# Performance work log

Measured on AMD Instinct MI355X. Metric: run time of the kernel, lower is better.

## Reference

```python
import jax, jax.numpy as jnp
import numpy as np

N_NODES = 100000
N_EDGES = 1600000
EMB = 64       # embedding_dim
HID = 128      # hidden_channels
N_GRAPHS = 512
N_TASKS = 128
ATOM_VOCAB = 119
BOND_VOCAB = 16


def setup_inputs() -> dict:
    key = jax.random.key(0)
    ks = jax.random.split(key, 24)
    s = 0.02
    inp = {
        'x_idx': jax.random.randint(ks[0], (N_NODES,), 0, ATOM_VOCAB),
        'edge_index': jax.random.randint(ks[1], (2, N_EDGES), 0, N_NODES),
        'edge_attr_idx': jax.random.randint(ks[2], (N_EDGES,), 0, BOND_VOCAB),
        'batch': jnp.sort(jax.random.randint(ks[3], (N_NODES,), 0, N_GRAPHS)),
        'atom_emb': jax.random.normal(ks[4], (ATOM_VOCAB, EMB), jnp.float32) * s,
        'bond_emb': jax.random.normal(ks[5], (BOND_VOCAB, EMB), jnp.float32) * s,
        'w_edge0': jax.random.normal(ks[6], (EMB, EMB), jnp.float32) * s,
        'b_edge0': jnp.zeros((EMB,), jnp.float32),
        'w1_0': jax.random.normal(ks[7], (EMB, HID), jnp.float32) * s,
        'b1_0': jnp.zeros((HID,), jnp.float32),
        'w2_0': jax.random.normal(ks[8], (HID, HID), jnp.float32) * s,
        'b2_0': jnp.zeros((HID,), jnp.float32),
        'w_edge1': jax.random.normal(ks[9], (EMB, HID), jnp.float32) * s,
        'b_edge1': jnp.zeros((HID,), jnp.float32),
        'w1_1': jax.random.normal(ks[10], (HID, HID), jnp.float32) * s,
        'b1_1': jnp.zeros((HID,), jnp.float32),
        'w2_1': jax.random.normal(ks[11], (HID, HID), jnp.float32) * s,
        'b2_1': jnp.zeros((HID,), jnp.float32),
        'lin1_w': jax.random.normal(ks[12], (HID, HID), jnp.float32) * s,
        'lin1_b': jnp.zeros((HID,), jnp.float32),
        'lin2_w': jax.random.normal(ks[13], (HID, N_TASKS), jnp.float32) * s,
        'lin2_b': jnp.zeros((N_TASKS,), jnp.float32),
    }
    return inp


def _gine_conv(x, e, src, dst, we, be, w1, b1, w2, b2):
    # message: relu(x_j + Linear(edge_attr)); aggregate: scatter-add at dst
    msg = jax.nn.relu(x[src] + e @ we + be)            # [E, in_dim]
    agg = jax.ops.segment_sum(msg, dst, num_segments=N_NODES)
    h = x + agg                                        # (1+eps)*x with eps=0
    h = jax.nn.elu(h @ w1 + b1) @ w2 + b2              # GINE nn MLP
    return jax.nn.elu(h)                               # outer F.elu


def reference(x_idx, edge_index, edge_attr_idx, batch,
              atom_emb, bond_emb,
              w_edge0, b_edge0, w1_0, b1_0, w2_0, b2_0,
              w_edge1, b_edge1, w1_1, b1_1, w2_1, b2_1,
              lin1_w, lin1_b, lin2_w, lin2_b):
    x = atom_emb[x_idx]                                # [N, EMB]
    e = bond_emb[edge_attr_idx]                        # [E, EMB]
    src, dst = edge_index[0], edge_index[1]            # flow: source->target
    x = _gine_conv(x, e, src, dst, w_edge0, b_edge0, w1_0, b1_0, w2_0, b2_0)
    x = _gine_conv(x, e, src, dst, w_edge1, b_edge1, w1_1, b1_1, w2_1, b2_1)
    hg = jax.ops.segment_sum(x, batch, num_segments=N_GRAPHS)  # global_add_pool
    hg = jax.nn.relu(hg @ lin1_w + lin1_b)
    return hg @ lin2_w + lin2_b                        # [G, num_tasks]
```

## Files before the change

### kernel.cpp

```cpp
#include <hip/hip_runtime.h>
#include <hip/hip_bf16.h>

static const int NN = 100000;
static const int NE = 1600000;
static const int NG = 512;
static const int NB = 391;
static const int PS = 4608;
static const int CS = 4624;

typedef __attribute__((ext_vector_type(8))) short shortx8;
typedef __attribute__((ext_vector_type(4))) float floatx4;
typedef __attribute__((ext_vector_type(2))) float floatx2;

__device__ __forceinline__ float bf2f(unsigned short u) {
  union { unsigned int i; float f; } v; v.i = ((unsigned int)u) << 16; return v.f;
}
__device__ __forceinline__ unsigned short f2bf(float f) {
  union { float f; unsigned int i; } v; v.f = f;
  return (unsigned short)((v.i + 0x7FFFu + ((v.i >> 16) & 1u)) >> 16);
}
__device__ __forceinline__ float elu_fast(float v) {
  return v > 0.f ? v : (__builtin_amdgcn_exp2f(v * 1.44269504f) - 1.f);
}
__device__ __forceinline__ floatx2 unpk(unsigned int v) {
  union { unsigned int i; float f; } a, b;
  a.i = v << 16; b.i = v & 0xFFFF0000u;
  floatx2 r; r.x = a.f; r.y = b.f; return r;
}

__global__ void k_prep(const float* __restrict__ bond,
                       const float* __restrict__ we0, const float* __restrict__ be0,
                       const float* __restrict__ we1, const float* __restrict__ be1,
                       const float* __restrict__ atom,
                       float* __restrict__ et1, unsigned short* __restrict__ M0,
                       float* __restrict__ hgf, int* __restrict__ bcursor,
                       const float* __restrict__ s0, const float* __restrict__ s1,
                       const float* __restrict__ s2, const float* __restrict__ s3,
                       const float* __restrict__ s4, const float* __restrict__ s5,
                       unsigned short* __restrict__ d0, unsigned short* __restrict__ d1,
                       unsigned short* __restrict__ d2, unsigned short* __restrict__ d3,
                       unsigned short* __restrict__ d4, unsigned short* __restrict__ d5) {
  int blk = blockIdx.x, t = threadIdx.x;
  if (blk < 8) {
    int i = blk * 256 + t;
    int b = i >> 7, c = i & 127;
    float acc = be1[c];
    for (int k = 0; k < 64; ++k) acc += bond[b * 64 + k] * we1[k * 128 + c];
    et1[i] = acc;
  } else if (blk < 484) {
    int i = (blk - 8) * 256 + t;
    int c = i & 63, b = (i >> 6) & 15, a = i >> 10;
    float acc = be0[c];
    for (int k = 0; k < 64; ++k) acc += bond[b * 64 + k] * we0[k * 64 + c];
    acc += atom[a * 64 + c];
    M0[i] = f2bf(acc > 0.f ? acc : 0.f);
  } else if (blk < 868) {
    int task = (blk - 484) >> 6;
    int i = ((blk - 484) & 63) * 256 + t;
    const float* w; unsigned short* wz; int K;
    switch (task) {
      case 0: w = s0; wz = d0; K = 64; break;
      case 1: w = s1; wz = d1; K = 128; break;
      case 2: w = s2; wz = d2; K = 128; break;
      case 3: w = s3; wz = d3; K = 128; break;
      case 4: w = s4; wz = d4; K = 128; break;
      default: w = s5; wz = d5; K = 128; break;
    }
    if (i >= K * 128) return;
    int j = i & 7, lane = (i >> 3) & 63, ct = (i >> 9) & 7, s = i >> 12;
    int k = s * 32 + (lane >> 4) * 8 + j;
    int m = ct * 16 + (lane & 15);
    wz[i] = f2bf(w[k * 128 + m]);
  } else if (blk < 884) {
    int base = (blk - 868) * 4096;
#pragma unroll
    for (int k = 0; k < 16; ++k) hgf[base + k * 256 + t] = 0.f;
  } else {
    if (t < NB) bcursor[t] = t * PS;
    int u = t + 256;
    if (u < NB) bcursor[u] = u * PS;
  }
}

__global__ void k_bin(const int* __restrict__ src, const int* __restrict__ dstp,
                      const int* __restrict__ ea, const int* __restrict__ x_idx,
                      int* __restrict__ bcursor, uint2* __restrict__ pairs) {
  __shared__ int cnt[512];
  __shared__ int incl[512];
  __shared__ int cur[NB];
  __shared__ int rbase[NB];
  __shared__ uint2 stage[2048];
  int t = threadIdx.x;
  int e0 = blockIdx.x * 2048;
  int ecnt = NE - e0; if (ecnt > 2048) ecnt = 2048;
  cnt[t] = 0; cnt[t + 256] = 0;
  __syncthreads();
  for (int k = 0; k < 8; ++k) {
    int i = k * 256 + t;
    if (i < ecnt) atomicAdd(&cnt[dstp[e0 + i] >> 8], 1);
  }
  __syncthreads();
  incl[t] = cnt[t]; incl[t + 256] = cnt[t + 256];
  __syncthreads();
  for (int d = 1; d < 512; d <<= 1) {
    int v0 = (t >= d) ? incl[t - d] : 0;
    int v1 = (t + 256 >= d) ? incl[t + 256 - d] : 0;
    __syncthreads();
    incl[t] += v0; incl[t + 256] += v1;
    __syncthreads();
  }
  if (t < NB) { cur[t] = incl[t] - cnt[t]; if (cnt[t]) rbase[t] = atomicAdd(&bcursor[t], cnt[t]); }
  int u = t + 256;
  if (u < NB) { cur[u] = incl[u] - cnt[u]; if (cnt[u]) rbase[u] = atomicAdd(&bcursor[u], cnt[u]); }
  __syncthreads();
  for (int k = 0; k < 8; ++k) {
    int i = k * 256 + t;
    if (i < ecnt) {
      int e = e0 + i;
      int d = dstp[e];
      int s = src[e];
      unsigned int pk = (unsigned int)s | ((unsigned int)(x_idx[s] * 16 + ea[e]) << 17);
      int p = atomicAdd(&cur[d >> 8], 1);
      stage[p] = make_uint2((unsigned int)d, pk);
    }
  }
  __syncthreads();
  for (int j = t; j < ecnt; j += 256) {
    uint2 p = stage[j];
    int b = (int)(p.x >> 8);
    int excl = incl[b] - cnt[b];
    pairs[rbase[b] + (j - excl)] = p;
  }
}

__global__ void k_fine(const uint2* __restrict__ pairs, const int* __restrict__ bcursor,
                       int* __restrict__ offs, int* __restrict__ cnts,
                       unsigned int* __restrict__ csr0, unsigned int* __restrict__ csr1) {
  __shared__ int cnt[256];
  __shared__ int incl[256];
  __shared__ int cur[256];
  int b = blockIdx.x;
  int t = threadIdx.x;
  int start = b * PS;
  int endv = bcursor[b];
  int cbase = b * CS;
  int base_n = b << 8;
  cnt[t] = 0;
  __syncthreads();
  for (int j = start + t; j < endv; j += 256)
    atomicAdd(&cnt[(int)pairs[j].x - base_n], 1);
  __syncthreads();
  incl[t] = cnt[t];
  __syncthreads();
  for (int d = 1; d < 256; d <<= 1) {
    int v = (t >= d) ? incl[t - d] : 0;
    __syncthreads();
    incl[t] += v;
    __syncthreads();
  }
  int excl = incl[t] - cnt[t];
  cur[t] = excl;
  int node = base_n + t;
  if (node < NN) { offs[node] = cbase + excl; cnts[node] = cnt[t]; }
  __syncthreads();
  for (int j = start + t; j < endv; j += 256) {
    uint2 p = pairs[j];
    int pos = cbase + atomicAdd(&cur[(int)p.x - base_n], 1);
    unsigned int pk = p.y;
    unsigned int idx17 = pk >> 17;
    csr0[pos] = idx17 << 7;
    csr1[pos] = ((pk & 0x1FFFFu) << 8) | (idx17 & 15u);
  }
  __syncthreads();
  int total = incl[255];
  if (t < 16) { csr0[cbase + total + t] = 0u; csr1[cbase + total + t] = 0u; }
}

__global__ __launch_bounds__(256) void k_agg0(
    const int* __restrict__ x_idx, const float* __restrict__ atom,
    const unsigned short* __restrict__ M0, const int* __restrict__ offs,
    const int* __restrict__ cnts,
    const unsigned int* __restrict__ csr0, unsigned short* __restrict__ h0) {
  int t = threadIdx.x, lane = t & 63;
  int half = lane >> 5, c = lane & 31;
  int n = __builtin_amdgcn_readfirstlane(blockIdx.x * 4 + (t >> 6));
  if (n >= NN) return;
  int s = offs[n], e = s + cnts[n];
  const char* Mb = (const char*)M0;
  unsigned int voff = (unsigned int)c * 4u;
  floatx2 acc; acc.x = 0.f; acc.y = 0.f;
  if (half == 0) {
    float2 sv = *(const float2*)((const char*)atom +
                                 ((size_t)(unsigned)x_idx[n] << 8) + (size_t)c * 8u);
    acc.x = sv.x; acc.y = sv.y;
  }
  for (int i = s; i < e; i += 16) {
    unsigned int a0 = csr0[i + 0],  b0 = csr0[i + 1];
    unsigned int a1 = csr0[i + 2],  b1 = csr0[i + 3];
    unsigned int a2 = csr0[i + 4],  b2 = csr0[i + 5];
    unsigned int a3 = csr0[i + 6],  b3 = csr0[i + 7];
    unsigned int a4 = csr0[i + 8],  b4 = csr0[i + 9];
    unsigned int a5 = csr0[i + 10], b5 = csr0[i + 11];
    unsigned int a6 = csr0[i + 12], b6 = csr0[i + 13];
    unsigned int a7 = csr0[i + 14], b7 = csr0[i + 15];
    unsigned int q0 = half ? b0 : a0, q1 = half ? b1 : a1;
    unsigned int q2 = half ? b2 : a2, q3 = half ? b3 : a3;
    unsigned int q4 = half ? b4 : a4, q5 = half ? b5 : a5;
    unsigned int q6 = half ? b6 : a6, q7 = half ? b7 : a7;
    floatx2 m0, m1, m2, m3, m4, m5, m6, m7;
    m0.x = m0.y = (i + 0 + half < e) ? 1.f : 0.f;
    m1.x = m1.y = (i + 2 + half < e) ? 1.f : 0.f;
    m2.x = m2.y = (i + 4 + half < e) ? 1.f : 0.f;
    m3.x = m3.y = (i + 6 + half < e) ? 1.f : 0.f;
    m4.x = m4.y = (i + 8 + half < e) ? 1.f : 0.f;
    m5.x = m5.y = (i + 10 + half < e) ? 1.f : 0.f;
    m6.x = m6.y = (i + 12 + half < e) ? 1.f : 0.f;
    m7.x = m7.y = (i + 14 + half < e) ? 1.f : 0.f;
    unsigned int v0 = *(const unsigned int*)(Mb + q0 + voff);
    unsigned int v1 = *(const unsigned int*)(Mb + q1 + voff);
    unsigned int v2 = *(const unsigned int*)(Mb + q2 + voff);
    unsigned int v3 = *(const unsigned int*)(Mb + q3 + voff);
    unsigned int v4 = *(const unsigned int*)(Mb + q4 + voff);
    unsigned int v5 = *(const unsigned int*)(Mb + q5 + voff);
    unsigned int v6 = *(const unsigned int*)(Mb + q6 + voff);
    unsigned int v7 = *(const unsigned int*)(Mb + q7 + voff);
    acc = __builtin_elementwise_fma(m0, unpk(v0), acc);
    acc = __builtin_elementwise_fma(m1, unpk(v1), acc);
    acc = __builtin_elementwise_fma(m2, unpk(v2), acc);
    acc = __builtin_elementwise_fma(m3, unpk(v3), acc);
    acc = __builtin_elementwise_fma(m4, unpk(v4), acc);
    acc = __builtin_elementwise_fma(m5, unpk(v5), acc);
    acc = __builtin_elementwise_fma(m6, unpk(v6), acc);
    acc = __builtin_elementwise_fma(m7, unpk(v7), acc);
  }
  float ax = acc.x + __shfl_xor(acc.x, 32);
  float ay = acc.y + __shfl_xor(acc.y, 32);
  if (half == 0) {
    unsigned int o = (unsigned int)f2bf(ax) | ((unsigned int)f2bf(ay) << 16);
    *(unsigned int*)(h0 + (size_t)n * 64 + c * 2) = o;
  }
}

__global__ __launch_bounds__(256) void k_agg1(
    const unsigned short* __restrict__ x1, const float* __restrict__ et1,
    const int* __restrict__ offs, const int* __restrict__ cnts,
    const unsigned int* __restrict__ csr1, unsigned short* __restrict__ h1) {
  __shared__ float etl[2048];
  int t = threadIdx.x;
#pragma unroll
  for (int k = 0; k < 8; ++k) etl[k * 256 + t] = et1[k * 256 + t];
  __syncthreads();
  int lane = t & 63;
  int n = __builtin_amdgcn_readfirstlane(blockIdx.x * 4 + (t >> 6));
  if (n >= NN) return;
  int s = offs[n], e = s + cnts[n];
  const char* xb = (const char*)x1;
  unsigned int voff = (unsigned int)lane * 4u;
  const char* etb = (const char*)etl + (size_t)lane * 8u;
  unsigned int xv = *(const unsigned int*)(xb + ((size_t)(unsigned)n << 8) + voff);
  floatx2 acc = unpk(xv);
  floatx2 zero2; zero2.x = 0.f; zero2.y = 0.f;
  for (int i = s; i < e; i += 8) {
    unsigned int q0 = csr1[i + 0], q1 = csr1[i + 1], q2 = csr1[i + 2], q3 = csr1[i + 3];
    unsigned int q4 = csr1[i + 4], q5 = csr1[i + 5], q6 = csr1[i + 6], q7 = csr1[i + 7];
    floatx2 k1, k2, k3, k4, k5, k6, k7;
    k1.x = k1.y = (i + 1 < e) ? 1.f : 0.f;
    k2.x = k2.y = (i + 2 < e) ? 1.f : 0.f;
    k3.x = k3.y = (i + 3 < e) ? 1.f : 0.f;
    k4.x = k4.y = (i + 4 < e) ? 1.f : 0.f;
    k5.x = k5.y = (i + 5 < e) ? 1.f : 0.f;
    k6.x = k6.y = (i + 6 < e) ? 1.f : 0.f;
    k7.x = k7.y = (i + 7 < e) ? 1.f : 0.f;
    unsigned int v0 = *(const unsigned int*)(xb + (q0 & 0xFFFFFF00u) + voff);
    unsigned int v1 = *(const unsigned int*)(xb + (q1 & 0xFFFFFF00u) + voff);
    unsigned int v2 = *(const unsigned int*)(xb + (q2 & 0xFFFFFF00u) + voff);
    unsigned int v3 = *(const unsigned int*)(xb + (q3 & 0xFFFFFF00u) + voff);
    unsigned int v4 = *(const unsigned int*)(xb + (q4 & 0xFFFFFF00u) + voff);
    unsigned int v5 = *(const unsigned int*)(xb + (q5 & 0xFFFFFF00u) + voff);
    unsigned int v6 = *(const unsigned int*)(xb + (q6 & 0xFFFFFF00u) + voff);
    unsigned int v7 = *(const unsigned int*)(xb + (q7 & 0xFFFFFF00u) + voff);
    floatx2 e0 = *(const floatx2*)(etb + ((q0 & 15u) << 9));
    floatx2 e1 = *(const floatx2*)(etb + ((q1 & 15u) << 9));
    floatx2 e2 = *(const floatx2*)(etb + ((q2 & 15u) << 9));
    floatx2 e3 = *(const floatx2*)(etb + ((q3 & 15u) << 9));
    floatx2 e4 = *(const floatx2*)(etb + ((q4 & 15u) << 9));
    floatx2 e5 = *(const floatx2*)(etb + ((q5 & 15u) << 9));
    floatx2 e6 = *(const floatx2*)(etb + ((q6 & 15u) << 9));
    floatx2 e7 = *(const floatx2*)(etb + ((q7 & 15u) << 9));
    acc = acc + __builtin_elementwise_max(unpk(v0) + e0, zero2);
    acc = __builtin_elementwise_fma(k1, __builtin_elementwise_max(unpk(v1) + e1, zero2), acc);
    acc = __builtin_elementwise_fma(k2, __builtin_elementwise_max(unpk(v2) + e2, zero2), acc);
    acc = __builtin_elementwise_fma(k3, __builtin_elementwise_max(unpk(v3) + e3, zero2), acc);
    acc = __builtin_elementwise_fma(k4, __builtin_elementwise_max(unpk(v4) + e4, zero2), acc);
    acc = __builtin_elementwise_fma(k5, __builtin_elementwise_max(unpk(v5) + e5, zero2), acc);
    acc = __builtin_elementwise_fma(k6, __builtin_elementwise_max(unpk(v6) + e6, zero2), acc);
    acc = __builtin_elementwise_fma(k7, __builtin_elementwise_max(unpk(v7) + e7, zero2), acc);
  }
  unsigned int o = (unsigned int)f2bf(acc.x) | ((unsigned int)f2bf(acc.y) << 16);
  *(unsigned int*)(h1 + (size_t)n * 128 + lane * 2) = o;
}

template <int K1>
__global__ __launch_bounds__(256) void k_mlp_t(
    const unsigned short* __restrict__ in,
    const unsigned short* __restrict__ w1z, const float* __restrict__ b1,
    const unsigned short* __restrict__ w2z, const float* __restrict__ b2,
    unsigned short* __restrict__ outb, int N) {
  __shared__ unsigned short tls[4][16][136];
  __shared__ unsigned short b2s[16384];
  int t = threadIdx.x;
  int lane = t & 63;
  int wave = t >> 6;
  int rlo = lane & 15, quad = lane >> 4;

#pragma unroll
  for (int k = 0; k < 8; ++k)
    *(shortx8*)&b2s[(k * 256 + t) * 8] = *(const shortx8*)&w2z[(k * 256 + t) * 8];

  float bm1[8], bm2[8];
#pragma unroll
  for (int ct = 0; ct < 8; ++ct) { bm1[ct] = b1[ct * 16 + rlo]; bm2[ct] = b2[ct * 16 + rlo]; }

  __syncthreads();

#pragma unroll
  for (int t2 = 0; t2 < 2; ++t2) {
    int row0 = blockIdx.x * 128 + t2 * 64 + wave * 16;
    int arow = row0 + rlo;

    floatx4 acc[8];
#pragma unroll
    for (int ct = 0; ct < 8; ++ct) { acc[ct][0]=0.f; acc[ct][1]=0.f; acc[ct][2]=0.f; acc[ct][3]=0.f; }
    const int NS = K1 >> 5;
#pragma unroll
    for (int s = 0; s < NS; ++s) {
      shortx8 a = {0,0,0,0,0,0,0,0};
      if (arow < N) a = *(const shortx8*)(in + (size_t)arow * K1 + s * 32 + quad * 8);
      const unsigned short* wp = w1z + ((size_t)(s * 8) * 64 + lane) * 8;
#pragma unroll
      for (int ct = 0; ct < 8; ++ct) {
        shortx8 b = *(const shortx8*)(wp + ct * 512);
        acc[ct] = __builtin_amdgcn_mfma_f32_16x16x32_bf16(a, b, acc[ct], 0, 0, 0);
      }
    }
#pragma unroll
    for (int ct = 0; ct < 8; ++ct) {
#pragma unroll
      for (int r = 0; r < 4; ++r) {
        float v = elu_fast(acc[ct][r] + bm1[ct]);
        tls[wave][quad * 4 + r][ct * 16 + rlo] = f2bf(v);
      }
    }

    floatx4 acc2[8];
#pragma unroll
    for (int ct = 0; ct < 8; ++ct) { acc2[ct][0]=0.f; acc2[ct][1]=0.f; acc2[ct][2]=0.f; acc2[ct][3]=0.f; }
#pragma unroll
    for (int s = 0; s < 4; ++s) {
      shortx8 a = *(const shortx8*)&tls[wave][rlo][s * 32 + quad * 8];
      const unsigned short* wp = &b2s[((s * 8) * 64 + lane) * 8];
#pragma unroll
      for (int ct = 0; ct < 8; ++ct) {
        shortx8 b = *(const shortx8*)(wp + ct * 512);
        acc2[ct] = __builtin_amdgcn_mfma_f32_16x16x32_bf16(a, b, acc2[ct], 0, 0, 0);
      }
    }
#pragma unroll
    for (int ct = 0; ct < 8; ++ct) {
#pragma unroll
      for (int r = 0; r < 4; ++r) {
        float v = elu_fast(acc2[ct][r] + bm2[ct]);
        tls[wave][quad * 4 + r][ct * 16 + rlo] = f2bf(v);
      }
    }
    int srow = lane >> 2;
    int schunk = lane & 3;
    int grow = row0 + srow;
#pragma unroll
    for (int k = 0; k < 4; ++k) {
      int ch = schunk + k * 4;
      if (grow < N)
        *(shortx8*)(outb + (size_t)grow * 128 + ch * 8) =
            *(const shortx8*)&tls[wave][srow][ch * 8];
    }
  }
}

__global__ __launch_bounds__(256) void k_pool(
    const unsigned short* __restrict__ x2, const int* __restrict__ batch,
    float* __restrict__ hgf) {
  int gt = blockIdx.x * 256 + threadIdx.x;
  int chunk = gt >> 6, lane = gt & 63;
  int n0 = chunk * 32;
  if (n0 >= NN) return;
  int nend = n0 + 32; if (nend > NN) nend = NN;
  float ax = 0.f, ay = 0.f;
  const unsigned short* xp = x2 + lane * 2;
  int gcur = batch[n0];
  for (int n = n0; n < nend; ++n) {
    int g = batch[n];
    if (g != gcur) {
      atomicAdd(&hgf[gcur * 128 + lane * 2], ax);
      atomicAdd(&hgf[gcur * 128 + lane * 2 + 1], ay);
      ax = 0.f; ay = 0.f; gcur = g;
    }
    unsigned int v = *(const unsigned int*)(xp + (size_t)n * 128);
    ax += bf2f((unsigned short)(v & 0xFFFF));
    ay += bf2f((unsigned short)(v >> 16));
  }
  atomicAdd(&hgf[gcur * 128 + lane * 2], ax);
  atomicAdd(&hgf[gcur * 128 + lane * 2 + 1], ay);
}

__global__ void k_head(const float* __restrict__ in,
                       const unsigned short* __restrict__ w1z, const float* __restrict__ b1,
                       const unsigned short* __restrict__ w2z, const float* __restrict__ b2,
                       float* __restrict__ outf, int N) {
  __shared__ unsigned short tls[4][16][136];
  int lane = threadIdx.x & 63;
  int wave = threadIdx.x >> 6;
  int row0 = blockIdx.x * 64 + wave * 16;
  int rlo = lane & 15, quad = lane >> 4;
  int arow = row0 + rlo;
  floatx4 acc[8];
#pragma unroll
  for (int ct = 0; ct < 8; ++ct) { acc[ct][0]=0.f; acc[ct][1]=0.f; acc[ct][2]=0.f; acc[ct][3]=0.f; }
#pragma unroll
  for (int s = 0; s < 4; ++s) {
    shortx8 a = {0,0,0,0,0,0,0,0};
    if (arow < N) {
      const float* rp = in + (size_t)arow * 128 + s * 32 + quad * 8;
      float4 f0 = *(const float4*)rp;
      float4 f1 = *(const float4*)(rp + 4);
      a[0] = (short)f2bf(f0.x); a[1] = (short)f2bf(f0.y);
      a[2] = (short)f2bf(f0.z); a[3] = (short)f2bf(f0.w);
      a[4] = (short)f2bf(f1.x); a[5] = (short)f2bf(f1.y);
      a[6] = (short)f2bf(f1.z); a[7] = (short)f2bf(f1.w);
    }
    const unsigned short* wp = w1z + ((size_t)(s * 8) * 64 + lane) * 8;
#pragma unroll
    for (int ct = 0; ct < 8; ++ct) {
      shortx8 b = *(const shortx8*)(wp + ct * 512);
      acc[ct] = __builtin_amdgcn_mfma_f32_16x16x32_bf16(a, b, acc[ct], 0, 0, 0);
    }
  }
#pragma unroll
  for (int ct = 0; ct < 8; ++ct) {
    float bm = b1[ct * 16 + rlo];
#pragma unroll
    for (int r = 0; r < 4; ++r) {
      float v = acc[ct][r] + bm;
      v = v > 0.f ? v : 0.f;
      tls[wave][quad * 4 + r][ct * 16 + rlo] = f2bf(v);
    }
  }
  __syncthreads();
  floatx4 acc2[8];
#pragma unroll
  for (int ct = 0; ct < 8; ++ct) { acc2[ct][0]=0.f; acc2[ct][1]=0.f; acc2[ct][2]=0.f; acc2[ct][3]=0.f; }
#pragma unroll
  for (int s = 0; s < 4; ++s) {
    shortx8 a = *(const shortx8*)&tls[wave][rlo][s * 32 + quad * 8];
    const unsigned short* wp = w2z + ((size_t)(s * 8) * 64 + lane) * 8;
#pragma unroll
    for (int ct = 0; ct < 8; ++ct) {
      shortx8 b = *(const shortx8*)(wp + ct * 512);
      acc2[ct] = __builtin_amdgcn_mfma_f32_16x16x32_bf16(a, b, acc2[ct], 0, 0, 0);
    }
  }
#pragma unroll
  for (int ct = 0; ct < 8; ++ct) {
    float bm = b2[ct * 16 + rlo];
#pragma unroll
    for (int r = 0; r < 4; ++r) {
      int rr = row0 + quad * 4 + r;
      if (rr < N) outf[(size_t)rr * 128 + ct * 16 + rlo] = acc2[ct][r] + bm;
    }
  }
}

extern "C" void kernel_launch(void* const* d_in, const int* in_sizes, int n_in,
                              void* d_out, int out_size, void* d_ws, size_t ws_size,
                              hipStream_t stream) {
  const int* x_idx  = (const int*)d_in[0];
  const int* e_src  = (const int*)d_in[1];
  const int* e_dst  = e_src + NE;
  const int* e_attr = (const int*)d_in[2];
  const int* batch  = (const int*)d_in[3];
  const float* atom = (const float*)d_in[4];
  const float* bond = (const float*)d_in[5];
  const float* we0  = (const float*)d_in[6];
  const float* be0  = (const float*)d_in[7];
  const float* w1_0 = (const float*)d_in[8];
  const float* b1_0 = (const float*)d_in[9];
  const float* w2_0 = (const float*)d_in[10];
  const float* b2_0 = (const float*)d_in[11];
  const float* we1  = (const float*)d_in[12];
  const float* be1  = (const float*)d_in[13];
  const float* w1_1 = (const float*)d_in[14];
  const float* b1_1 = (const float*)d_in[15];
  const float* w2_1 = (const float*)d_in[16];
  const float* b2_1 = (const float*)d_in[17];
  const float* l1w  = (const float*)d_in[18];
  const float* l1b  = (const float*)d_in[19];
  const float* l2w  = (const float*)d_in[20];
  const float* l2b  = (const float*)d_in[21];

  char* ws = (char*)d_ws;
  size_t off = 0;
  auto alloc = [&](size_t bytes) -> void* {
    void* p = ws + off;
    off = (off + bytes + 255) & ~(size_t)255;
    return p;
  };
  int* bcursor = (int*)alloc((size_t)NB * 4);
  int* offs    = (int*)alloc((size_t)NN * 4);
  int* cnts    = (int*)alloc((size_t)NN * 4);
  float* et1   = (float*)alloc(16 * 128 * 4);
  unsigned short* M0 = (unsigned short*)alloc((size_t)1904 * 64 * 2);
  float* hgf   = (float*)alloc((size_t)NG * 128 * 4);
  unsigned short* w1_0z = (unsigned short*)alloc(64 * 128 * 2);
  unsigned short* w2_0z = (unsigned short*)alloc(128 * 128 * 2);
  unsigned short* w1_1z = (unsigned short*)alloc(128 * 128 * 2);
  unsigned short* w2_1z = (unsigned short*)alloc(128 * 128 * 2);
  unsigned short* l1z   = (unsigned short*)alloc(128 * 128 * 2);
  unsigned short* l2z   = (unsigned short*)alloc(128 * 128 * 2);
  uint2* pairs = (uint2*)alloc((size_t)NB * PS * 8);
  unsigned int* csr0 = (unsigned int*)alloc((size_t)NB * CS * 4);
  unsigned int* csr1 = (unsigned int*)alloc((size_t)NB * CS * 4);
  unsigned short* x1 = (unsigned short*)alloc((size_t)NN * 128 * 2);
  unsigned short* h1 = (unsigned short*)alloc((size_t)NN * 128 * 2);
  unsigned short* h0 = (unsigned short*)pairs;
  unsigned short* x2 = h1;

  k_prep<<<885, 256, 0, stream>>>(bond, we0, be0, we1, be1, atom, et1, M0, hgf, bcursor,
                                  w1_0, w2_0, w1_1, w2_1, l1w, l2w,
                                  w1_0z, w2_0z, w1_1z, w2_1z, l1z, l2z);
  k_bin<<<(NE + 2047) / 2048, 256, 0, stream>>>(e_src, e_dst, e_attr, x_idx, bcursor, pairs);
  k_fine<<<NB, 256, 0, stream>>>(pairs, bcursor, offs, cnts, csr0, csr1);
  k_agg0<<<NN / 4, 256, 0, stream>>>(x_idx, atom, M0, offs, cnts, csr0, h0);
  k_mlp_t<64><<<(NN + 127) / 128, 256, 0, stream>>>(h0, w1_0z, b1_0, w2_0z, b2_0, x1, NN);
  k_agg1<<<NN / 4, 256, 0, stream>>>(x1, et1, offs, cnts, csr1, h1);
  k_mlp_t<128><<<(NN + 127) / 128, 256, 0, stream>>>(h1, w1_1z, b1_1, w2_1z, b2_1, x2, NN);
  k_pool<<<(((NN + 31) / 32) * 64 + 255) / 256, 256, 0, stream>>>(x2, batch, hgf);
  k_head<<<(NG + 63) / 64, 256, 0, stream>>>(hgf, l1z, l1b, l2z, l2b, (float*)d_out, NG);
}
```

Measured before the change: 333.8 us.

## Replace two-level binned CSR build with global count, scan, and atomic scatter

The CSR construction changes. The old version had a bucket-binning pass into an intermediate pairs buffer followed by a per-bucket fine sort. The new version counts in-degrees with global atomics inside the prep kernel, computes per-bucket offsets with a block scan, and scatters edges directly into the CSR with per-node global atomic cursors. This removes the intermediate pairs write and read and one pass over the edges. In exchange it adds two memsets and many contended global atomics with random scattered writes, and edge order within each node's list becomes nondeterministic.

New measurement: 433.0 us. 1.3x slower.

```diff
diff --git a/kernel.cpp b/kernel.cpp
--- a/kernel.cpp
+++ b/kernel.cpp
@@ -5,7 +5,6 @@
 static const int NE = 1600000;
 static const int NG = 512;
 static const int NB = 391;
-static const int PS = 4608;
 static const int CS = 4624;
 
 typedef __attribute__((ext_vector_type(8))) short shortx8;
@@ -33,7 +32,8 @@
                        const float* __restrict__ we1, const float* __restrict__ be1,
                        const float* __restrict__ atom,
                        float* __restrict__ et1, unsigned short* __restrict__ M0,
-                       float* __restrict__ hgf, int* __restrict__ bcursor,
+                       float* __restrict__ hgf,
+                       const int* __restrict__ dstp, int* __restrict__ cnt,
                        const float* __restrict__ s0, const float* __restrict__ s1,
                        const float* __restrict__ s2, const float* __restrict__ s3,
                        const float* __restrict__ s4, const float* __restrict__ s5,
@@ -76,81 +76,22 @@
 #pragma unroll
     for (int k = 0; k < 16; ++k) hgf[base + k * 256 + t] = 0.f;
   } else {
-    if (t < NB) bcursor[t] = t * PS;
-    int u = t + 256;
-    if (u < NB) bcursor[u] = u * PS;
-  }
-}
-
-__global__ void k_bin(const int* __restrict__ src, const int* __restrict__ dstp,
-                      const int* __restrict__ ea, const int* __restrict__ x_idx,
-                      int* __restrict__ bcursor, uint2* __restrict__ pairs) {
-  __shared__ int cnt[512];
-  __shared__ int incl[512];
-  __shared__ int cur[NB];
-  __shared__ int rbase[NB];
-  __shared__ uint2 stage[2048];
-  int t = threadIdx.x;
-  int e0 = blockIdx.x * 2048;
-  int ecnt = NE - e0; if (ecnt > 2048) ecnt = 2048;
-  cnt[t] = 0; cnt[t + 256] = 0;
-  __syncthreads();
-  for (int k = 0; k < 8; ++k) {
-    int i = k * 256 + t;
-    if (i < ecnt) atomicAdd(&cnt[dstp[e0 + i] >> 8], 1);
-  }
-  __syncthreads();
-  incl[t] = cnt[t]; incl[t + 256] = cnt[t + 256];
-  __syncthreads();
-  for (int d = 1; d < 512; d <<= 1) {
-    int v0 = (t >= d) ? incl[t - d] : 0;
-    int v1 = (t + 256 >= d) ? incl[t + 256 - d] : 0;
-    __syncthreads();
-    incl[t] += v0; incl[t + 256] += v1;
-    __syncthreads();
-  }
-  if (t < NB) { cur[t] = incl[t] - cnt[t]; if (cnt[t]) rbase[t] = atomicAdd(&bcursor[t], cnt[t]); }
-  int u = t + 256;
-  if (u < NB) { cur[u] = incl[u] - cnt[u]; if (cnt[u]) rbase[u] = atomicAdd(&bcursor[u], cnt[u]); }
-  __syncthreads();
-  for (int k = 0; k < 8; ++k) {
-    int i = k * 256 + t;
-    if (i < ecnt) {
-      int e = e0 + i;
-      int d = dstp[e];
-      int s = src[e];
-      unsigned int pk = (unsigned int)s | ((unsigned int)(x_idx[s] * 16 + ea[e]) << 17);
-      int p = atomicAdd(&cur[d >> 8], 1);
-      stage[p] = make_uint2((unsigned int)d, pk);
-    }
-  }
-  __syncthreads();
-  for (int j = t; j < ecnt; j += 256) {
-    uint2 p = stage[j];
-    int b = (int)(p.x >> 8);
-    int excl = incl[b] - cnt[b];
-    pairs[rbase[b] + (j - excl)] = p;
-  }
-}
-
-__global__ void k_fine(const uint2* __restrict__ pairs, const int* __restrict__ bcursor,
-                       int* __restrict__ offs, int* __restrict__ cnts,
+    int base = (blk - 884) * 2048;
+#pragma unroll
+    for (int k = 0; k < 8; ++k) {
+      int e = base + k * 256 + t;
+      if (e < NE) atomicAdd(&cnt[dstp[e]], 1);
+    }
+  }
+}
+
+__global__ void k_offs(const int* __restrict__ cnt, int* __restrict__ offs,
                        unsigned int* __restrict__ csr0, unsigned int* __restrict__ csr1) {
-  __shared__ int cnt[256];
   __shared__ int incl[256];
-  __shared__ int cur[256];
-  int b = blockIdx.x;
-  int t = threadIdx.x;
-  int start = b * PS;
-  int endv = bcursor[b];
-  int cbase = b * CS;
-  int base_n = b << 8;
-  cnt[t] = 0;
-  __syncthreads();
-  for (int j = start + t; j < endv; j += 256)
-    atomicAdd(&cnt[(int)pairs[j].x - base_n], 1);
-  __syncthreads();
-  incl[t] = cnt[t];
+  int b = blockIdx.x, t = threadIdx.x;
+  int node = (b << 8) + t;
+  int myc = (node < NN) ? cnt[node] : 0;
+  incl[t] = myc;
   __syncthreads();
   for (int d = 1; d < 256; d <<= 1) {
     int v = (t >= d) ? incl[t - d] : 0;
@@ -158,22 +99,30 @@
     incl[t] += v;
     __syncthreads();
   }
-  int excl = incl[t] - cnt[t];
-  cur[t] = excl;
-  int node = base_n + t;
-  if (node < NN) { offs[node] = cbase + excl; cnts[node] = cnt[t]; }
-  __syncthreads();
-  for (int j = start + t; j < endv; j += 256) {
-    uint2 p = pairs[j];
-    int pos = cbase + atomicAdd(&cur[(int)p.x - base_n], 1);
-    unsigned int pk = p.y;
-    unsigned int idx17 = pk >> 17;
-    csr0[pos] = idx17 << 7;
-    csr1[pos] = ((pk & 0x1FFFFu) << 8) | (idx17 & 15u);
-  }
-  __syncthreads();
+  int excl = incl[t] - myc;
+  int cbase = b * CS;
+  if (node < NN) offs[node] = cbase + excl;
   int total = incl[255];
   if (t < 16) { csr0[cbase + total + t] = 0u; csr1[cbase + total + t] = 0u; }
+}
+
+__global__ void k_scatter(const int* __restrict__ srcp, const int* __restrict__ dstp,
+                          const int* __restrict__ ea, const int* __restrict__ x_idx,
+                          const int* __restrict__ offs, int* __restrict__ cur,
+                          unsigned int* __restrict__ csr0, unsigned int* __restrict__ csr1) {
+  int base = blockIdx.x * 1024, t = threadIdx.x;
+#pragma unroll
+  for (int k = 0; k < 4; ++k) {
+    int e = base + k * 256 + t;
+    if (e < NE) {
+      int d = dstp[e];
+      int s = srcp[e];
+      unsigned int idx17 = (unsigned int)(x_idx[s] * 16 + ea[e]);
+      int pos = offs[d] + atomicAdd(&cur[d], 1);
+      csr0[pos] = idx17 << 7;
+      csr1[pos] = (((unsigned int)s) << 8) | (idx17 & 15u);
+    }
+  }
 }
 
 __global__ __launch_bounds__(256) void k_agg0(
@@ -513,9 +462,9 @@
     off = (off + bytes + 255) & ~(size_t)255;
     return p;
   };
-  int* bcursor = (int*)alloc((size_t)NB * 4);
+  int* cnt     = (int*)alloc((size_t)NN * 4);
+  int* cur     = (int*)alloc((size_t)NN * 4);
   int* offs    = (int*)alloc((size_t)NN * 4);
-  int* cnts    = (int*)alloc((size_t)NN * 4);
   float* et1   = (float*)alloc(16 * 128 * 4);
   unsigned short* M0 = (unsigned short*)alloc((size_t)1904 * 64 * 2);
   float* hgf   = (float*)alloc((size_t)NG * 128 * 4);
@@ -525,22 +474,25 @@
   unsigned short* w2_1z = (unsigned short*)alloc(128 * 128 * 2);
   unsigned short* l1z   = (unsigned short*)alloc(128 * 128 * 2);
   unsigned short* l2z   = (unsigned short*)alloc(128 * 128 * 2);
-  uint2* pairs = (uint2*)alloc((size_t)NB * PS * 8);
   unsigned int* csr0 = (unsigned int*)alloc((size_t)NB * CS * 4);
   unsigned int* csr1 = (unsigned int*)alloc((size_t)NB * CS * 4);
   unsigned short* x1 = (unsigned short*)alloc((size_t)NN * 128 * 2);
   unsigned short* h1 = (unsigned short*)alloc((size_t)NN * 128 * 2);
-  unsigned short* h0 = (unsigned short*)pairs;
+  unsigned short* h0 = (unsigned short*)alloc((size_t)NN * 64 * 2);
   unsigned short* x2 = h1;
 
-  k_prep<<<885, 256, 0, stream>>>(bond, we0, be0, we1, be1, atom, et1, M0, hgf, bcursor,
-                                  w1_0, w2_0, w1_1, w2_1, l1w, l2w,
-                                  w1_0z, w2_0z, w1_1z, w2_1z, l1z, l2z);
-  k_bin<<<(NE + 2047) / 2048, 256, 0, stream>>>(e_src, e_dst, e_attr, x_idx, bcursor, pairs);
-  k_fine<<<NB, 256, 0, stream>>>(pairs, bcursor, offs, cnts, csr0, csr1);
-  k_agg0<<<NN / 4, 256, 0, stream>>>(x_idx, atom, M0, offs, cnts, csr0, h0);
+  hipMemsetAsync(cnt, 0, (size_t)NN * 4, stream);
+  hipMemsetAsync(cur, 0, (size_t)NN * 4, stream);
+  k_prep<<<1666, 256, 0, stream>>>(bond, we0, be0, we1, be1, atom, et1, M0, hgf,
+                                   e_dst, cnt,
+                                   w1_0, w2_0, w1_1, w2_1, l1w, l2w,
+                                   w1_0z, w2_0z, w1_1z, w2_1z, l1z, l2z);
+  k_offs<<<NB, 256, 0, stream>>>(cnt, offs, csr0, csr1);
+  k_scatter<<<(NE + 1023) / 1024, 256, 0, stream>>>(e_src, e_dst, e_attr, x_idx,
+                                                    offs, cur, csr0, csr1);
+  k_agg0<<<NN / 4, 256, 0, stream>>>(x_idx, atom, M0, offs, cnt, csr0, h0);
   k_mlp_t<64><<<(NN + 127) / 128, 256, 0, stream>>>(h0, w1_0z, b1_0, w2_0z, b2_0, x1, NN);
-  k_agg1<<<NN / 4, 256, 0, stream>>>(x1, et1, offs, cnts, csr1, h1);
+  k_agg1<<<NN / 4, 256, 0, stream>>>(x1, et1, offs, cnt, csr1, h1);
   k_mlp_t<128><<<(NN + 127) / 128, 256, 0, stream>>>(h1, w1_1z, b1_1, w2_1z, b2_1, x2, NN);
   k_pool<<<(((NN + 31) / 32) * 64 + 255) / 256, 256, 0, stream>>>(x2, batch, hgf);
   k_head<<<(NG + 63) / 64, 256, 0, stream>>>(hgf, l1z, l1b, l2z, l2b, (float*)d_out, NG);
```
